# Optimization experiments

Hardware: AMD Instinct MI355X
Metric: run time of the kernel (lower is better)

Reference implementation:

```python
import jax, jax.numpy as jnp
import numpy as np

ALPHA = 0.25
GAMMA = 2.0
EPS = 1e-4
AREA_THR = 100.0  # 10*10


def calc_iou(a, b):
    # a: anchors [A,4] in (y1,x1,y2,x2); b: boxes [M,4] in (x1,y1,x2,y2)
    area = (b[:, 2] - b[:, 0]) * (b[:, 3] - b[:, 1])  # [M]
    iw = jnp.minimum(a[:, 3:4], b[None, :, 2]) - jnp.maximum(a[:, 1:2], b[None, :, 0])
    ih = jnp.minimum(a[:, 2:3], b[None, :, 3]) - jnp.maximum(a[:, 0:1], b[None, :, 1])
    iw = jnp.clip(iw, 0.0)
    ih = jnp.clip(ih, 0.0)
    ua = (a[:, 2] - a[:, 0])[:, None] * (a[:, 3] - a[:, 1])[:, None] + area[None, :] - iw * ih
    ua = jnp.clip(ua, 1e-8)
    return iw * ih / ua  # [A,M]


def setup_inputs() -> dict:
    key = jax.random.key(0)
    k1, k2, k3, k4, k5, k6, k7 = jax.random.split(key, 7)
    B, M, A, C = 8, 64, 49104, 80
    # GT boxes (x1,y1,x2,y2), well-formed
    xy = jax.random.uniform(k1, (B, M, 2), minval=0.0, maxval=400.0)
    wh = jax.random.uniform(k2, (B, M, 2), minval=10.0, maxval=100.0)
    boxes = jnp.concatenate([xy, xy + wh], axis=-1)
    labels = jax.random.randint(k3, (B, M), 0, C + 1)  # 0 = ignore
    # anchors (y1,x1,y2,x2), well-formed
    ac = jax.random.uniform(k4, (A, 2), minval=0.0, maxval=512.0)
    ahw = jax.random.uniform(k5, (A, 2), minval=16.0, maxval=128.0)
    anchors = jnp.concatenate([ac - 0.5 * ahw, ac + 0.5 * ahw], axis=-1)[None]  # [1,A,4]
    classification = jax.random.uniform(k6, (B, A, C), minval=0.0, maxval=1.0)
    regression = jax.random.normal(k7, (B, A, 4), dtype=jnp.float32)
    return {"boxes": boxes, "labels": labels, "anchors": anchors,
            "classification": classification, "regression": regression}


def _per_image(cls_j, reg_j, box_j, lab_j, anc, aw, ah, acx, acy):
    C = cls_j.shape[-1]
    valid = lab_j != 0  # [M]
    cls = jnp.clip(cls_j, EPS, 1.0 - EPS)
    iou = calc_iou(anc, box_j)                      # [A,M]
    iou = jnp.where(valid[None, :], iou, -1.0)      # mask padded GT
    iou_max = iou.max(axis=1)                       # [A]
    iou_arg = iou.argmax(axis=1)                    # [A]
    ab = box_j[iou_arg]                             # [A,4] assigned boxes
    al = lab_j[iou_arg] - 1                         # [A] assigned labels
    big = (ab[:, 2] - ab[:, 0]) * (ab[:, 3] - ab[:, 1]) > AREA_THR
    pos = (big & (iou_max >= 0.5)) | (~big & (iou_max >= 0.15))  # [A]
    npos = pos.sum().astype(cls.dtype)
    targets = jax.nn.one_hot(al, C, dtype=cls.dtype) * pos[:, None].astype(cls.dtype)
    is_one = targets == 1.0
    alpha_f = jnp.where(is_one, ALPHA, 1.0 - ALPHA)
    focal_w = alpha_f * jnp.where(is_one, 1.0 - cls, cls) ** GAMMA
    bce = -(targets * jnp.log(cls) + (1.0 - targets) * jnp.log(1.0 - cls))
    cls_loss = (focal_w * bce).sum() / jnp.maximum(npos, 1.0)
    gw = ab[:, 2] - ab[:, 0]
    gh = ab[:, 3] - ab[:, 1]
    gcx = ab[:, 0] + 0.5 * gw
    gcy = ab[:, 1] + 0.5 * gh
    gw = jnp.clip(gw, 1.0)
    gh = jnp.clip(gh, 1.0)
    t = jnp.stack([(gcy - acy) / ah, (gcx - acx) / aw,
                   jnp.log(gh / ah), jnp.log(gw / aw)], axis=1)  # [A,4] (dy,dx,dh,dw)
    diff = jnp.abs(t - reg_j)
    rl = jnp.where(diff <= 1.0 / 9.0, 0.5 * 9.0 * diff ** 2, diff - 0.5 / 9.0)
    reg_sum = (rl * pos[:, None].astype(cls.dtype)).sum()
    reg_loss = jnp.where(npos > 0, reg_sum / (4.0 * jnp.maximum(npos, 1.0)), 0.0)
    return cls_loss, reg_loss


def reference(boxes, labels, anchors, classification, regression):
    anc = anchors[0]  # [A,4] (y1,x1,y2,x2)
    aw = anc[:, 3] - anc[:, 1]
    ah = anc[:, 2] - anc[:, 0]
    acx = anc[:, 1] + 0.5 * aw
    acy = anc[:, 0] + 0.5 * ah
    cls_l, reg_l = jax.vmap(_per_image, in_axes=(0, 0, 0, 0, None, None, None, None, None))(
        classification, regression, boxes, labels, anc, aw, ah, acx, acy)
    cls_loss = cls_l.mean(keepdims=True)
    det_loss = reg_l.mean(keepdims=True) * 50.0
    return cls_loss, det_loss
```

## Files before the change

kernel.cpp:

```cpp
#include <hip/hip_runtime.h>

#define NB 8
#define NM 64
#define NA 49104
#define NC 80
#define EPSF 1e-4f
#define BPI 256
#define APB 192

struct Ws {
    float cnp[NB][BPI];
    float regp[NB][BPI];
    float npp[NB][BPI];
};

__device__ __forceinline__ float waveReduceSumF(float v) {
    #pragma unroll
    for (int off = 32; off > 0; off >>= 1) v += __shfl_down(v, off, 64);
    return v;
}

#define NEG_SCALE (-0.51986038542f)

#define CONSUME4(V)                                                   \
    s0 = fmaf((V).x * (V).x, __log2f(fmaxf(1.0f - (V).x, EPSF)), s0); \
    s1 = fmaf((V).y * (V).y, __log2f(fmaxf(1.0f - (V).y, EPSF)), s1); \
    s2 = fmaf((V).z * (V).z, __log2f(fmaxf(1.0f - (V).z, EPSF)), s2); \
    s3 = fmaf((V).w * (V).w, __log2f(fmaxf(1.0f - (V).w, EPSF)), s3);

__device__ __forceinline__ void anchorWork(int j, int a, float4 an,
                                           const float4* __restrict__ boxes4,
                                           const int* __restrict__ labels,
                                           const float* __restrict__ cls,
                                           const float4* __restrict__ reg,
                                           float& corr, float& regl, float& npf) {
    const int jb = j * NM;
    const float ay1 = an.x, ax1 = an.y, ay2 = an.z, ax2 = an.w;
    const float aare = (ay2 - ay1) * (ax2 - ax1);

    float best = -1.0f;
    int bi = 0;
    #pragma unroll 16
    for (int m = 0; m < NM; ++m) {
        const float4 bm = boxes4[jb + m];
        const int lab = labels[jb + m];
        const float bar = (bm.z - bm.x) * (bm.w - bm.y);
        const float bar_eff = (lab != 0) ? bar : __builtin_inff();
        float iw = fmaxf(fminf(ax2, bm.z) - fmaxf(ax1, bm.x), 0.0f);
        float ih = fmaxf(fminf(ay2, bm.w) - fmaxf(ay1, bm.y), 0.0f);
        float inter = iw * ih;
        float ua = (aare + bar_eff) - inter;
        float iou = inter * __builtin_amdgcn_rcpf(ua);
        bool upd = iou > best;
        best = upd ? iou : best;
        bi   = upd ? m : bi;
    }

    float4 bb = boxes4[jb + bi];
    int labg = labels[jb + bi];
    const float bar = (bb.z - bb.x) * (bb.w - bb.y);
    const bool big = bar > 100.0f;
    const float thr = big ? 0.5f : 0.15f;
    const bool pos = best >= thr;
    if (pos) {
        npf = 1.0f;
        const int al = labg - 1;
        float p = cls[((size_t)j * NA + a) * NC + al];
        p = fminf(fmaxf(p, EPSF), 1.0f - EPSF);
        const float om = 1.0f - p;
        corr = 0.25f * om * om * (-__logf(p)) - 0.75f * p * p * (-__logf(om));

        const float aw = ax2 - ax1, ah = ay2 - ay1;
        const float acx = ax1 + 0.5f * aw, acy = ay1 + 0.5f * ah;
        float gw = bb.z - bb.x;
        float gh = bb.w - bb.y;
        const float gcx = bb.x + 0.5f * gw;
        const float gcy = bb.y + 0.5f * gh;
        gw = fmaxf(gw, 1.0f);
        gh = fmaxf(gh, 1.0f);
        float4 r = reg[(size_t)j * NA + a];
        const float t0 = (gcy - acy) / ah;
        const float t1 = (gcx - acx) / aw;
        const float t2 = __logf(gh / ah);
        const float t3 = __logf(gw / aw);
        const float d0 = fabsf(t0 - r.x);
        const float d1 = fabsf(t1 - r.y);
        const float d2 = fabsf(t2 - r.z);
        const float d3 = fabsf(t3 - r.w);
        const float ninth = 1.0f / 9.0f;
        const float c = 0.5f / 9.0f;
        regl  = (d0 <= ninth) ? 4.5f * d0 * d0 : d0 - c;
        regl += (d1 <= ninth) ? 4.5f * d1 * d1 : d1 - c;
        regl += (d2 <= ninth) ? 4.5f * d2 * d2 : d2 - c;
        regl += (d3 <= ninth) ? 4.5f * d3 * d3 : d3 - c;
    }
}

__global__ void main_kernel(const float4* __restrict__ cls4,
                            const float* __restrict__ cls,
                            const float4* __restrict__ anchors4,
                            const float4* __restrict__ reg,
                            const float4* __restrict__ boxes4,
                            const int* __restrict__ labels,
                            Ws* __restrict__ ws) {
    const int j = blockIdx.y;
    const int bx = blockIdx.x;
    const int tid = threadIdx.x;

    const int per4 = NA * NC / 4;
    const int stride = BPI * 256;
    const float4* base = cls4 + (size_t)j * per4;
    const int b = bx * 256 + tid;
    const int a = bx * APB + tid;
    const int ai = a < NA ? a : NA - 1;

    float4 an = anchors4[ai];
    float4 nv0 = base[b];
    float4 nv1 = base[b + stride];

    float corr = 0.0f, regl = 0.0f, npf = 0.0f;
    if (tid < APB && a < NA)
        anchorWork(j, a, an, boxes4, labels, cls, reg, corr, regl, npf);

    float s0 = 0.0f, s1 = 0.0f, s2 = 0.0f, s3 = 0.0f;
    {
        float4 v = nv0, vn = nv1;
        #pragma unroll
        for (int k = 0; k < 14; ++k) {
            float4 nx;
            if (k < 12) nx = base[b + (k + 2) * stride];
            CONSUME4(v);
            v = vn; vn = nx;
        }
        if (b < per4 - 14 * stride) {
            float4 vt = base[b + 14 * stride];
            CONSUME4(vt);
        }
    }
    float cn = fmaf(NEG_SCALE, (s0 + s1) + (s2 + s3), corr);

    __shared__ float sred[3][4];
    cn   = waveReduceSumF(cn);
    regl = waveReduceSumF(regl);
    npf  = waveReduceSumF(npf);
    const int wid = tid >> 6;
    if ((tid & 63) == 0) {
        sred[0][wid] = cn; sred[1][wid] = regl; sred[2][wid] = npf;
    }
    __syncthreads();
    if (tid == 0) {
        ws->cnp[j][bx]  = sred[0][0] + sred[0][1] + sred[0][2] + sred[0][3];
        ws->regp[j][bx] = sred[1][0] + sred[1][1] + sred[1][2] + sred[1][3];
        ws->npp[j][bx]  = sred[2][0] + sred[2][1] + sred[2][2] + sred[2][3];
    }
}

__global__ void finalize_kernel(const Ws* __restrict__ ws, float* __restrict__ out) {
    __shared__ float scls[NB], sreg[NB];
    const int w = threadIdx.x >> 6;
    const int lane = threadIdx.x & 63;
    float cs = 0.0f, rs = 0.0f, np = 0.0f;
    #pragma unroll
    for (int i = lane; i < BPI; i += 64) {
        cs += ws->cnp[w][i];
        rs += ws->regp[w][i];
        np += ws->npp[w][i];
    }
    cs = waveReduceSumF(cs);
    rs = waveReduceSumF(rs);
    np = waveReduceSumF(np);
    if (lane == 0) {
        float d = fmaxf(np, 1.0f);
        scls[w] = cs / d;
        sreg[w] = (np > 0.0f) ? rs / (4.0f * d) : 0.0f;
    }
    __syncthreads();
    if (threadIdx.x == 0) {
        float acc = 0.0f, bsum = 0.0f;
        #pragma unroll
        for (int jj = 0; jj < NB; ++jj) { acc += scls[jj]; bsum += sreg[jj]; }
        out[0] = acc / (float)NB;
        out[1] = (bsum / (float)NB) * 50.0f;
    }
}

extern "C" void kernel_launch(void* const* d_in, const int* in_sizes, int n_in,
                              void* d_out, int out_size, void* d_ws, size_t ws_size,
                              hipStream_t stream) {
    const float* boxes   = (const float*)d_in[0];
    const int*   labels  = (const int*)d_in[1];
    const float* anchors = (const float*)d_in[2];
    const float* cls     = (const float*)d_in[3];
    const float* reg     = (const float*)d_in[4];
    float* out = (float*)d_out;
    Ws* ws = (Ws*)d_ws;

    dim3 g(BPI, NB);
    main_kernel<<<g, 256, 0, stream>>>((const float4*)cls, cls,
                                       (const float4*)anchors, (const float4*)reg,
                                       (const float4*)boxes, labels, ws);

    finalize_kernel<<<1, 512, 0, stream>>>(ws, out);
}
```

Before: 34.17 us.

## Interleave IoU box loop with streaming classification loads to hide latency

Moves the 64-box IoU argmax loop inside the 14-step streamed focal-loss loop, doing about five boxes per step, and issues the tail load up front. The aim is to overlap the IoU ALU work with the memory latency of the classification-tensor loads, which before ran only after the anchor work had finished. The per-iteration divergent branch for doA and the extra live registers could lower occupancy or add overhead.

After: 37.06 us. 1.08x slower.

```diff
diff --git a/kernel.cpp b/kernel.cpp
--- a/kernel.cpp
+++ b/kernel.cpp
@@ -28,74 +28,6 @@
     s2 = fmaf((V).z * (V).z, __log2f(fmaxf(1.0f - (V).z, EPSF)), s2); \
     s3 = fmaf((V).w * (V).w, __log2f(fmaxf(1.0f - (V).w, EPSF)), s3);
 
-__device__ __forceinline__ void anchorWork(int j, int a, float4 an,
-                                           const float4* __restrict__ boxes4,
-                                           const int* __restrict__ labels,
-                                           const float* __restrict__ cls,
-                                           const float4* __restrict__ reg,
-                                           float& corr, float& regl, float& npf) {
-    const int jb = j * NM;
-    const float ay1 = an.x, ax1 = an.y, ay2 = an.z, ax2 = an.w;
-    const float aare = (ay2 - ay1) * (ax2 - ax1);
-
-    float best = -1.0f;
-    int bi = 0;
-    #pragma unroll 16
-    for (int m = 0; m < NM; ++m) {
-        const float4 bm = boxes4[jb + m];
-        const int lab = labels[jb + m];
-        const float bar = (bm.z - bm.x) * (bm.w - bm.y);
-        const float bar_eff = (lab != 0) ? bar : __builtin_inff();
-        float iw = fmaxf(fminf(ax2, bm.z) - fmaxf(ax1, bm.x), 0.0f);
-        float ih = fmaxf(fminf(ay2, bm.w) - fmaxf(ay1, bm.y), 0.0f);
-        float inter = iw * ih;
-        float ua = (aare + bar_eff) - inter;
-        float iou = inter * __builtin_amdgcn_rcpf(ua);
-        bool upd = iou > best;
-        best = upd ? iou : best;
-        bi   = upd ? m : bi;
-    }
-
-    float4 bb = boxes4[jb + bi];
-    int labg = labels[jb + bi];
-    const float bar = (bb.z - bb.x) * (bb.w - bb.y);
-    const bool big = bar > 100.0f;
-    const float thr = big ? 0.5f : 0.15f;
-    const bool pos = best >= thr;
-    if (pos) {
-        npf = 1.0f;
-        const int al = labg - 1;
-        float p = cls[((size_t)j * NA + a) * NC + al];
-        p = fminf(fmaxf(p, EPSF), 1.0f - EPSF);
-        const float om = 1.0f - p;
-        corr = 0.25f * om * om * (-__logf(p)) - 0.75f * p * p * (-__logf(om));
-
-        const float aw = ax2 - ax1, ah = ay2 - ay1;
-        const float acx = ax1 + 0.5f * aw, acy = ay1 + 0.5f * ah;
-        float gw = bb.z - bb.x;
-        float gh = bb.w - bb.y;
-        const float gcx = bb.x + 0.5f * gw;
-        const float gcy = bb.y + 0.5f * gh;
-        gw = fmaxf(gw, 1.0f);
-        gh = fmaxf(gh, 1.0f);
-        float4 r = reg[(size_t)j * NA + a];
-        const float t0 = (gcy - acy) / ah;
-        const float t1 = (gcx - acx) / aw;
-        const float t2 = __logf(gh / ah);
-        const float t3 = __logf(gw / aw);
-        const float d0 = fabsf(t0 - r.x);
-        const float d1 = fabsf(t1 - r.y);
-        const float d2 = fabsf(t2 - r.z);
-        const float d3 = fabsf(t3 - r.w);
-        const float ninth = 1.0f / 9.0f;
-        const float c = 0.5f / 9.0f;
-        regl  = (d0 <= ninth) ? 4.5f * d0 * d0 : d0 - c;
-        regl += (d1 <= ninth) ? 4.5f * d1 * d1 : d1 - c;
-        regl += (d2 <= ninth) ? 4.5f * d2 * d2 : d2 - c;
-        regl += (d3 <= ninth) ? 4.5f * d3 * d3 : d3 - c;
-    }
-}
-
 __global__ void main_kernel(const float4* __restrict__ cls4,
                             const float* __restrict__ cls,
                             const float4* __restrict__ anchors4,
@@ -113,28 +45,91 @@
     const int b = bx * 256 + tid;
     const int a = bx * APB + tid;
     const int ai = a < NA ? a : NA - 1;
+    const int jb = j * NM;
+    const bool doA = (tid < APB) && (a < NA);
 
     float4 an = anchors4[ai];
-    float4 nv0 = base[b];
-    float4 nv1 = base[b + stride];
+    float4 q0 = base[b];
+    float4 q1 = base[b + stride];
+    const bool tail = b < per4 - 14 * stride;
+    float4 vt;
+    if (tail) vt = base[b + 14 * stride];
+
+    const float ay1 = an.x, ax1 = an.y, ay2 = an.z, ax2 = an.w;
+    const float aare = (ay2 - ay1) * (ax2 - ax1);
+    float best = -1.0f;
+    int bi = 0;
+
+    float s0 = 0.0f, s1 = 0.0f, s2 = 0.0f, s3 = 0.0f;
+
+    #pragma unroll
+    for (int k = 0; k < 14; ++k) {
+        float4 nx = q1;
+        if (k < 12) nx = base[b + (k + 2) * stride];
+        if (doA) {
+            #pragma unroll
+            for (int mm = 0; mm < 5; ++mm) {
+                const int m = k * 5 + mm;
+                if (m < NM) {
+                    const float4 bm = boxes4[jb + m];
+                    const int lab = labels[jb + m];
+                    const float bar = (bm.z - bm.x) * (bm.w - bm.y);
+                    const float bar_eff = (lab != 0) ? bar : __builtin_inff();
+                    float iw = fmaxf(fminf(ax2, bm.z) - fmaxf(ax1, bm.x), 0.0f);
+                    float ih = fmaxf(fminf(ay2, bm.w) - fmaxf(ay1, bm.y), 0.0f);
+                    float inter = iw * ih;
+                    float ua = (aare + bar_eff) - inter;
+                    float iou = inter * __builtin_amdgcn_rcpf(ua);
+                    bool upd = iou > best;
+                    best = upd ? iou : best;
+                    bi   = upd ? m : bi;
+                }
+            }
+        }
+        CONSUME4(q0);
+        q0 = q1; q1 = nx;
+    }
+    if (tail) { CONSUME4(vt); }
 
     float corr = 0.0f, regl = 0.0f, npf = 0.0f;
-    if (tid < APB && a < NA)
-        anchorWork(j, a, an, boxes4, labels, cls, reg, corr, regl, npf);
+    if (doA) {
+        float4 bb = boxes4[jb + bi];
+        int labg = labels[jb + bi];
+        const float bar = (bb.z - bb.x) * (bb.w - bb.y);
+        const bool big = bar > 100.0f;
+        const float thr = big ? 0.5f : 0.15f;
+        const bool pos = best >= thr;
+        if (pos) {
+            npf = 1.0f;
+            const int al = labg - 1;
+            float p = cls[((size_t)j * NA + a) * NC + al];
+            p = fminf(fmaxf(p, EPSF), 1.0f - EPSF);
+            const float om = 1.0f - p;
+            corr = 0.25f * om * om * (-__logf(p)) - 0.75f * p * p * (-__logf(om));
 
-    float s0 = 0.0f, s1 = 0.0f, s2 = 0.0f, s3 = 0.0f;
-    {
-        float4 v = nv0, vn = nv1;
-        #pragma unroll
-        for (int k = 0; k < 14; ++k) {
-            float4 nx;
-            if (k < 12) nx = base[b + (k + 2) * stride];
-            CONSUME4(v);
-            v = vn; vn = nx;
-        }
-        if (b < per4 - 14 * stride) {
-            float4 vt = base[b + 14 * stride];
-            CONSUME4(vt);
+            const float aw = ax2 - ax1, ah = ay2 - ay1;
+            const float acx = ax1 + 0.5f * aw, acy = ay1 + 0.5f * ah;
+            float gw = bb.z - bb.x;
+            float gh = bb.w - bb.y;
+            const float gcx = bb.x + 0.5f * gw;
+            const float gcy = bb.y + 0.5f * gh;
+            gw = fmaxf(gw, 1.0f);
+            gh = fmaxf(gh, 1.0f);
+            float4 r = reg[(size_t)j * NA + a];
+            const float t0 = (gcy - acy) / ah;
+            const float t1 = (gcx - acx) / aw;
+            const float t2 = __logf(gh / ah);
+            const float t3 = __logf(gw / aw);
+            const float d0 = fabsf(t0 - r.x);
+            const float d1 = fabsf(t1 - r.y);
+            const float d2 = fabsf(t2 - r.z);
+            const float d3 = fabsf(t3 - r.w);
+            const float ninth = 1.0f / 9.0f;
+            const float c = 0.5f / 9.0f;
+            regl  = (d0 <= ninth) ? 4.5f * d0 * d0 : d0 - c;
+            regl += (d1 <= ninth) ? 4.5f * d1 * d1 : d1 - c;
+            regl += (d2 <= ninth) ? 4.5f * d2 * d2 : d2 - c;
+            regl += (d3 <= ninth) ? 4.5f * d3 * d3 : d3 - c;
         }
     }
     float cn = fmaf(NEG_SCALE, (s0 + s1) + (s2 + s3), corr);
```

## Split anchor matching and classification streaming into separate block roles

Applied to the files above, without the earlier changes.

Blocks are now specialized: the first 192 blocks per image do IoU matching and positive-anchor losses with all 256 threads, and the next 256 blocks stream the classification tensor for the negative focal term. Previously every block did both, with 192 of 256 threads running the 64-box IoU loop before starting the bandwidth-bound stream, which serialized compute and memory inside each wave. Specialization lets compute-heavy and memory-heavy blocks run concurrently across CUs. In exchange the grid grows from 256 to 448 blocks per image, and the finalize kernel reads more partials.

Result: slower. 37.67 us (+10.3%).

```diff
diff --git a/kernel.cpp b/kernel.cpp
--- a/kernel.cpp
+++ b/kernel.cpp
@@ -5,13 +5,14 @@
 #define NA 49104
 #define NC 80
 #define EPSF 1e-4f
-#define BPI 256
-#define APB 192
+#define ANCB 192
+#define STRB 256
 
 struct Ws {
-    float cnp[NB][BPI];
-    float regp[NB][BPI];
-    float npp[NB][BPI];
+    float negp[NB][STRB];
+    float corrp[NB][ANCB];
+    float regp[NB][ANCB];
+    float npp[NB][ANCB];
 };
 
 __device__ __forceinline__ float waveReduceSumF(float v) {
@@ -27,74 +28,6 @@
     s1 = fmaf((V).y * (V).y, __log2f(fmaxf(1.0f - (V).y, EPSF)), s1); \
     s2 = fmaf((V).z * (V).z, __log2f(fmaxf(1.0f - (V).z, EPSF)), s2); \
     s3 = fmaf((V).w * (V).w, __log2f(fmaxf(1.0f - (V).w, EPSF)), s3);
-
-__device__ __forceinline__ void anchorWork(int j, int a, float4 an,
-                                           const float4* __restrict__ boxes4,
-                                           const int* __restrict__ labels,
-                                           const float* __restrict__ cls,
-                                           const float4* __restrict__ reg,
-                                           float& corr, float& regl, float& npf) {
-    const int jb = j * NM;
-    const float ay1 = an.x, ax1 = an.y, ay2 = an.z, ax2 = an.w;
-    const float aare = (ay2 - ay1) * (ax2 - ax1);
-
-    float best = -1.0f;
-    int bi = 0;
-    #pragma unroll 16
-    for (int m = 0; m < NM; ++m) {
-        const float4 bm = boxes4[jb + m];
-        const int lab = labels[jb + m];
-        const float bar = (bm.z - bm.x) * (bm.w - bm.y);
-        const float bar_eff = (lab != 0) ? bar : __builtin_inff();
-        float iw = fmaxf(fminf(ax2, bm.z) - fmaxf(ax1, bm.x), 0.0f);
-        float ih = fmaxf(fminf(ay2, bm.w) - fmaxf(ay1, bm.y), 0.0f);
-        float inter = iw * ih;
-        float ua = (aare + bar_eff) - inter;
-        float iou = inter * __builtin_amdgcn_rcpf(ua);
-        bool upd = iou > best;
-        best = upd ? iou : best;
-        bi   = upd ? m : bi;
-    }
-
-    float4 bb = boxes4[jb + bi];
-    int labg = labels[jb + bi];
-    const float bar = (bb.z - bb.x) * (bb.w - bb.y);
-    const bool big = bar > 100.0f;
-    const float thr = big ? 0.5f : 0.15f;
-    const bool pos = best >= thr;
-    if (pos) {
-        npf = 1.0f;
-        const int al = labg - 1;
-        float p = cls[((size_t)j * NA + a) * NC + al];
-        p = fminf(fmaxf(p, EPSF), 1.0f - EPSF);
-        const float om = 1.0f - p;
-        corr = 0.25f * om * om * (-__logf(p)) - 0.75f * p * p * (-__logf(om));
-
-        const float aw = ax2 - ax1, ah = ay2 - ay1;
-        const float acx = ax1 + 0.5f * aw, acy = ay1 + 0.5f * ah;
-        float gw = bb.z - bb.x;
-        float gh = bb.w - bb.y;
-        const float gcx = bb.x + 0.5f * gw;
-        const float gcy = bb.y + 0.5f * gh;
-        gw = fmaxf(gw, 1.0f);
-        gh = fmaxf(gh, 1.0f);
-        float4 r = reg[(size_t)j * NA + a];
-        const float t0 = (gcy - acy) / ah;
-        const float t1 = (gcx - acx) / aw;
-        const float t2 = __logf(gh / ah);
-        const float t3 = __logf(gw / aw);
-        const float d0 = fabsf(t0 - r.x);
-        const float d1 = fabsf(t1 - r.y);
-        const float d2 = fabsf(t2 - r.z);
-        const float d3 = fabsf(t3 - r.w);
-        const float ninth = 1.0f / 9.0f;
-        const float c = 0.5f / 9.0f;
-        regl  = (d0 <= ninth) ? 4.5f * d0 * d0 : d0 - c;
-        regl += (d1 <= ninth) ? 4.5f * d1 * d1 : d1 - c;
-        regl += (d2 <= ninth) ? 4.5f * d2 * d2 : d2 - c;
-        regl += (d3 <= ninth) ? 4.5f * d3 * d3 : d3 - c;
-    }
-}
 
 __global__ void main_kernel(const float4* __restrict__ cls4,
                             const float* __restrict__ cls,
@@ -106,25 +39,94 @@
     const int j = blockIdx.y;
     const int bx = blockIdx.x;
     const int tid = threadIdx.x;
-
-    const int per4 = NA * NC / 4;
-    const int stride = BPI * 256;
-    const float4* base = cls4 + (size_t)j * per4;
-    const int b = bx * 256 + tid;
-    const int a = bx * APB + tid;
-    const int ai = a < NA ? a : NA - 1;
-
-    float4 an = anchors4[ai];
-    float4 nv0 = base[b];
-    float4 nv1 = base[b + stride];
-
-    float corr = 0.0f, regl = 0.0f, npf = 0.0f;
-    if (tid < APB && a < NA)
-        anchorWork(j, a, an, boxes4, labels, cls, reg, corr, regl, npf);
-
-    float s0 = 0.0f, s1 = 0.0f, s2 = 0.0f, s3 = 0.0f;
-    {
-        float4 v = nv0, vn = nv1;
+    __shared__ float sred[3][4];
+
+    if (bx < ANCB) {
+        const int a = bx * 256 + tid;
+        const bool doA = a < NA;
+        const int jb = j * NM;
+        float4 an = anchors4[doA ? a : NA - 1];
+        const float ay1 = an.x, ax1 = an.y, ay2 = an.z, ax2 = an.w;
+        const float aare = (ay2 - ay1) * (ax2 - ax1);
+
+        float best = -1.0f;
+        int bi = 0;
+        #pragma unroll 16
+        for (int m = 0; m < NM; ++m) {
+            const float4 bm = boxes4[jb + m];
+            const int lab = labels[jb + m];
+            const float bar = (bm.z - bm.x) * (bm.w - bm.y);
+            const float bar_eff = (lab != 0) ? bar : __builtin_inff();
+            float iw = fmaxf(fminf(ax2, bm.z) - fmaxf(ax1, bm.x), 0.0f);
+            float ih = fmaxf(fminf(ay2, bm.w) - fmaxf(ay1, bm.y), 0.0f);
+            float inter = iw * ih;
+            float ua = (aare + bar_eff) - inter;
+            float iou = inter * __builtin_amdgcn_rcpf(ua);
+            bool upd = iou > best;
+            best = upd ? iou : best;
+            bi   = upd ? m : bi;
+        }
+
+        float corr = 0.0f, regl = 0.0f, npf = 0.0f;
+        if (doA) {
+            float4 bb = boxes4[jb + bi];
+            int labg = labels[jb + bi];
+            const float bar = (bb.z - bb.x) * (bb.w - bb.y);
+            const float thr = (bar > 100.0f) ? 0.5f : 0.15f;
+            if (best >= thr) {
+                npf = 1.0f;
+                const int al = labg - 1;
+                float p = cls[((size_t)j * NA + a) * NC + al];
+                p = fminf(fmaxf(p, EPSF), 1.0f - EPSF);
+                const float om = 1.0f - p;
+                corr = 0.25f * om * om * (-__logf(p)) - 0.75f * p * p * (-__logf(om));
+
+                const float aw = ax2 - ax1, ah = ay2 - ay1;
+                const float acx = ax1 + 0.5f * aw, acy = ay1 + 0.5f * ah;
+                float gw = bb.z - bb.x, gh = bb.w - bb.y;
+                const float gcx = bb.x + 0.5f * gw, gcy = bb.y + 0.5f * gh;
+                gw = fmaxf(gw, 1.0f);
+                gh = fmaxf(gh, 1.0f);
+                float4 r = reg[(size_t)j * NA + a];
+                const float t0 = (gcy - acy) / ah;
+                const float t1 = (gcx - acx) / aw;
+                const float t2 = __logf(gh / ah);
+                const float t3 = __logf(gw / aw);
+                const float d0 = fabsf(t0 - r.x);
+                const float d1 = fabsf(t1 - r.y);
+                const float d2 = fabsf(t2 - r.z);
+                const float d3 = fabsf(t3 - r.w);
+                const float ninth = 1.0f / 9.0f;
+                const float c = 0.5f / 9.0f;
+                regl  = (d0 <= ninth) ? 4.5f * d0 * d0 : d0 - c;
+                regl += (d1 <= ninth) ? 4.5f * d1 * d1 : d1 - c;
+                regl += (d2 <= ninth) ? 4.5f * d2 * d2 : d2 - c;
+                regl += (d3 <= ninth) ? 4.5f * d3 * d3 : d3 - c;
+            }
+        }
+        corr = waveReduceSumF(corr);
+        regl = waveReduceSumF(regl);
+        npf  = waveReduceSumF(npf);
+        const int wid = tid >> 6;
+        if ((tid & 63) == 0) {
+            sred[0][wid] = corr; sred[1][wid] = regl; sred[2][wid] = npf;
+        }
+        __syncthreads();
+        if (tid == 0) {
+            ws->corrp[j][bx] = sred[0][0] + sred[0][1] + sred[0][2] + sred[0][3];
+            ws->regp[j][bx]  = sred[1][0] + sred[1][1] + sred[1][2] + sred[1][3];
+            ws->npp[j][bx]   = sred[2][0] + sred[2][1] + sred[2][2] + sred[2][3];
+        }
+    } else {
+        const int sbx = bx - ANCB;
+        const int per4 = NA * NC / 4;
+        const int stride = STRB * 256;
+        const float4* base = cls4 + (size_t)j * per4;
+        const int b = sbx * 256 + tid;
+
+        float4 v = base[b];
+        float4 vn = base[b + stride];
+        float s0 = 0.0f, s1 = 0.0f, s2 = 0.0f, s3 = 0.0f;
         #pragma unroll
         for (int k = 0; k < 14; ++k) {
             float4 nx;
@@ -136,22 +138,14 @@
             float4 vt = base[b + 14 * stride];
             CONSUME4(vt);
         }
-    }
-    float cn = fmaf(NEG_SCALE, (s0 + s1) + (s2 + s3), corr);
-
-    __shared__ float sred[3][4];
-    cn   = waveReduceSumF(cn);
-    regl = waveReduceSumF(regl);
-    npf  = waveReduceSumF(npf);
-    const int wid = tid >> 6;
-    if ((tid & 63) == 0) {
-        sred[0][wid] = cn; sred[1][wid] = regl; sred[2][wid] = npf;
-    }
-    __syncthreads();
-    if (tid == 0) {
-        ws->cnp[j][bx]  = sred[0][0] + sred[0][1] + sred[0][2] + sred[0][3];
-        ws->regp[j][bx] = sred[1][0] + sred[1][1] + sred[1][2] + sred[1][3];
-        ws->npp[j][bx]  = sred[2][0] + sred[2][1] + sred[2][2] + sred[2][3];
+        float negs = NEG_SCALE * ((s0 + s1) + (s2 + s3));
+
+        negs = waveReduceSumF(negs);
+        const int wid = tid >> 6;
+        if ((tid & 63) == 0) sred[0][wid] = negs;
+        __syncthreads();
+        if (tid == 0)
+            ws->negp[j][sbx] = sred[0][0] + sred[0][1] + sred[0][2] + sred[0][3];
     }
 }
 
@@ -159,19 +153,22 @@
     __shared__ float scls[NB], sreg[NB];
     const int w = threadIdx.x >> 6;
     const int lane = threadIdx.x & 63;
-    float cs = 0.0f, rs = 0.0f, np = 0.0f;
+    float ns = 0.0f, cs = 0.0f, rs = 0.0f, np = 0.0f;
     #pragma unroll
-    for (int i = lane; i < BPI; i += 64) {
-        cs += ws->cnp[w][i];
+    for (int i = lane; i < STRB; i += 64) ns += ws->negp[w][i];
+    #pragma unroll
+    for (int i = lane; i < ANCB; i += 64) {
+        cs += ws->corrp[w][i];
         rs += ws->regp[w][i];
         np += ws->npp[w][i];
     }
+    ns = waveReduceSumF(ns);
     cs = waveReduceSumF(cs);
     rs = waveReduceSumF(rs);
     np = waveReduceSumF(np);
     if (lane == 0) {
         float d = fmaxf(np, 1.0f);
-        scls[w] = cs / d;
+        scls[w] = (ns + cs) / d;
         sreg[w] = (np > 0.0f) ? rs / (4.0f * d) : 0.0f;
     }
     __syncthreads();
@@ -195,7 +192,7 @@
     float* out = (float*)d_out;
     Ws* ws = (Ws*)d_ws;
 
-    dim3 g(BPI, NB);
+    dim3 g(ANCB + STRB, NB);
     main_kernel<<<g, 256, 0, stream>>>((const float4*)cls, cls,
                                        (const float4*)anchors, (const float4*)reg,
                                        (const float4*)boxes, labels, ws);
```
